# Kernel optimization log

Measured on AMD Instinct MI355X. Metric: run time of the kernel, lower is better.

## Reference

```python
import jax, jax.numpy as jnp
import numpy as np

SEQ_LEN, N_VARS, N_SKILLS, D_IN = 120, 9, 32, 1
BATCH = 32768


def setup_inputs() -> dict:
    key = jax.random.key(0)
    ks = jax.random.split(key, 8)
    H, D = N_SKILLS, D_IN
    s = 1.0 / np.sqrt(H)  # torch LSTMCell init scale
    return {
        "x": jax.random.normal(ks[0], (BATCH, N_VARS * SEQ_LEN), dtype=jnp.float32),
        # nn.LSTMCell params (gate order i,f,g,o)
        "W_ih": jax.random.uniform(ks[1], (4 * H, D), jnp.float32, -s, s),
        "W_hh": jax.random.uniform(ks[2], (4 * H, H), jnp.float32, -s, s),
        "b_ih": jax.random.uniform(ks[3], (4 * H,), jnp.float32, -s, s),
        "b_hh": jax.random.uniform(ks[4], (4 * H,), jnp.float32, -s, s),
        # contextual gate params: cg_w Linear(D,H,bias=False), cg_u Linear(H,H)
        "cg_w": jax.random.uniform(ks[5], (H, D), jnp.float32, -s, s),
        "cg_u": jax.random.uniform(ks[6], (H, H), jnp.float32, -s, s),
        "cg_b": jax.random.uniform(ks[7], (H,), jnp.float32, -s, s),
    }


def reference(x, W_ih, W_hh, b_ih, b_hh, cg_w, cg_u, cg_b):
    B = x.shape[0]
    H = N_SKILLS
    # [B, V*T] -> fold the 9 independent variable-sequences into the batch dim
    # (the same cell weights are shared across vars), then scan over time.
    xs = x.reshape(B * N_VARS, SEQ_LEN, D_IN)
    xs = jnp.moveaxis(xs, 1, 0)  # [T, B*V, D_IN]

    def step(carry, xt):
        h, c = carry  # each [B*V, H]
        gates = xt @ W_ih.T + b_ih + h @ W_hh.T + b_hh  # [B*V, 4H]
        i, f, g, o = jnp.split(gates, 4, axis=-1)
        i = jax.nn.sigmoid(i)
        f = jax.nn.sigmoid(f)
        g = jnp.tanh(g)
        c_new = f * c + i * g
        # contextual gate uses the *previous* h
        cg = jax.nn.sigmoid(xt @ cg_w.T + h @ cg_u.T + cg_b)
        h_new = cg * jnp.tanh(c_new)
        return (h_new, c_new), None

    zeros = jnp.zeros((B * N_VARS, H), dtype=x.dtype)
    (h, _), _ = jax.lax.scan(step, (zeros, zeros), xs)
    # [B*V, H] -> [B, V*H] (variable-major, matching torch.cat over vars)
    return h.reshape(B, N_VARS * H)
```

## Files before the change

### kernel.cpp

```cpp
#include <hip/hip_runtime.h>


#define NV 9
#define TLEN 120
#define HS 32
#define BATCH_ 32768
#define NSEQ (BATCH_ * NV)
#define NBATCH (NSEQ / 16)
#define WPB 4
#define GRID_ (NBATCH / (WPB * 2))

#define TCHUNK 60
#define XSTRIDE 20
#define HSTRIDE 36

#define LOG2E 1.4426950408889634f
#define TWOL  2.8853900817779268f

typedef __attribute__((ext_vector_type(8))) short bf16x8;
typedef __attribute__((ext_vector_type(4))) float f32x4;
typedef __attribute__((ext_vector_type(4))) unsigned int u32x4;

__device__ __forceinline__ float fast_exp2(float x) { return __builtin_amdgcn_exp2f(x); }
__device__ __forceinline__ float fast_rcp(float x)  { return __builtin_amdgcn_rcpf(x); }
__device__ __forceinline__ unsigned int fbits(float x) { return __builtin_bit_cast(unsigned int, x); }
__device__ __forceinline__ float bcastf(unsigned int x) { return __builtin_bit_cast(float, x); }

__device__ __forceinline__ f32x4 splat4(float x) { f32x4 v = {x, x, x, x}; return v; }
__device__ __forceinline__ f32x4 fma4(f32x4 a, f32x4 b, f32x4 c) {
  return __builtin_elementwise_fma(a, b, c);
}
__device__ __forceinline__ f32x4 exp24(f32x4 v) {
  f32x4 r;
  r[0] = fast_exp2(v[0]); r[1] = fast_exp2(v[1]);
  r[2] = fast_exp2(v[2]); r[3] = fast_exp2(v[3]);
  return r;
}
__device__ __forceinline__ f32x4 rcp4(f32x4 v) {
  f32x4 r;
  r[0] = fast_rcp(v[0]); r[1] = fast_rcp(v[1]);
  r[2] = fast_rcp(v[2]); r[3] = fast_rcp(v[3]);
  return r;
}

__device__ __forceinline__ void lstm_elem(f32x4 ai, f32x4 af, f32x4 ag, f32x4 ac,
                                          f32x4& ct, f32x4& h) {
  const f32x4 one4 = splat4(1.0f);
  f32x4 Ei = exp24(ai), Ef = exp24(af), Eg = exp24(ag), Ea = exp24(ac);
  f32x4 pi_ = Ei + one4, pf_ = Ef + one4, pg_ = Eg + one4, pa_ = Ea + one4;
  f32x4 u   = fma4(Eg, splat4(TWOL), splat4(-TWOL));
  f32x4 P   = pi_ * pg_;
  f32x4 tt  = pf_ * u;
  f32x4 num = fma4(ct, P, tt);
  f32x4 den = pf_ * P;
  ct = num * rcp4(den);
  f32x4 Ec  = exp24(ct);
  h = (one4 - Ec) * rcp4(pa_ * (Ec + one4));
}

__device__ __forceinline__ void gates8(const unsigned int* __restrict__ hb,
                                       const float* __restrict__ xTw, int tl,
                                       int col, int quad,
                                       const bf16x8 (&bhi)[8], const bf16x8 (&blo)[8],
                                       const float (&wx)[8], const float (&bb)[8],
                                       f32x4 (&acc)[8]) {
  f32x4 xt4 = *(const f32x4*)&xTw[tl * XSTRIDE + quad * 4];
#pragma unroll
  for (int tile = 0; tile < 8; ++tile)
    acc[tile] = fma4(splat4(wx[tile]), xt4, splat4(bb[tile]));
  const unsigned int* hrow = &hb[col * HSTRIDE + quad * 8];
  u32x4 wa = *(const u32x4*)hrow;
  u32x4 wz = *(const u32x4*)(hrow + 4);
  u32x4 hi4, lo4;
  hi4[0] = __builtin_amdgcn_perm(wa[1], wa[0], 0x05040100u);
  hi4[1] = __builtin_amdgcn_perm(wa[3], wa[2], 0x05040100u);
  hi4[2] = __builtin_amdgcn_perm(wz[1], wz[0], 0x05040100u);
  hi4[3] = __builtin_amdgcn_perm(wz[3], wz[2], 0x05040100u);
  lo4[0] = __builtin_amdgcn_perm(wa[1], wa[0], 0x07060302u);
  lo4[1] = __builtin_amdgcn_perm(wa[3], wa[2], 0x07060302u);
  lo4[2] = __builtin_amdgcn_perm(wz[1], wz[0], 0x07060302u);
  lo4[3] = __builtin_amdgcn_perm(wz[3], wz[2], 0x07060302u);
  bf16x8 ahi = __builtin_bit_cast(bf16x8, hi4);
  bf16x8 alo = __builtin_bit_cast(bf16x8, lo4);
#pragma unroll
  for (int tile = 0; tile < 8; ++tile) {
    acc[tile] = __builtin_amdgcn_mfma_f32_16x16x32_bf16(ahi, bhi[tile], acc[tile], 0, 0, 0);
    acc[tile] = __builtin_amdgcn_mfma_f32_16x16x32_bf16(alo, bhi[tile], acc[tile], 0, 0, 0);
    acc[tile] = __builtin_amdgcn_mfma_f32_16x16x32_bf16(ahi, blo[tile], acc[tile], 0, 0, 0);
  }
}

__device__ __forceinline__ void finish8(unsigned int* __restrict__ hb, int col, int quad,
                                        f32x4 (&acc)[8],
                                        f32x4& ct0, f32x4& ct1, f32x4& h0, f32x4& h1) {
  lstm_elem(acc[0], acc[2], acc[4], acc[6], ct0, h0);
  lstm_elem(acc[1], acc[3], acc[5], acc[7], ct1, h1);
#pragma unroll
  for (int r = 0; r < 4; ++r) {
    unsigned int hbits = fbits(h0[r]);
    float lof = h0[r] - bcastf(hbits & 0xffff0000u);
    hb[(quad * 4 + r) * HSTRIDE + col] =
        __builtin_amdgcn_perm(fbits(lof), hbits, 0x07060302u);
    unsigned int hbits1 = fbits(h1[r]);
    float lof1 = h1[r] - bcastf(hbits1 & 0xffff0000u);
    hb[(quad * 4 + r) * HSTRIDE + col + 16] =
        __builtin_amdgcn_perm(fbits(lof1), hbits1, 0x07060302u);
  }
}

__global__ __launch_bounds__(256, 2) void cglstm_kernel(
    const float* __restrict__ x,
    const float* __restrict__ W_ih,
    const float* __restrict__ W_hh,
    const float* __restrict__ b_ih,
    const float* __restrict__ b_hh,
    const float* __restrict__ cg_w,
    const float* __restrict__ cg_u,
    const float* __restrict__ cg_b,
    float* __restrict__ out)
{
  const int lane = threadIdx.x & 63;
  const int wid  = threadIdx.x >> 6;
  const int col  = lane & 15;
  const int quad = lane >> 4;

  __shared__ __align__(16) float xT[WPB][2][TCHUNK * XSTRIDE];
  __shared__ __align__(16) unsigned int hbuf[WPB][2][16 * HSTRIDE];
  float* __restrict__ xTw0 = xT[wid][0];
  float* __restrict__ xTw1 = xT[wid][1];
  unsigned int* hb0 = hbuf[wid][0];
  unsigned int* hb1 = hbuf[wid][1];

  bf16x8 bhi[8], blo[8];
  float wx[8], bb[8];
#pragma unroll
  for (int tile = 0; tile < 8; ++tile) {
    const int n = col + (tile & 1) * 16;
    const float sc_ = ((tile >> 1) == 2) ? -TWOL : -LOG2E;
    const float* wrow = (tile < 6) ? (W_hh + (size_t)((tile >> 1) * HS + n) * HS)
                                   : (cg_u + (size_t)n * HS);
    bf16x8 vh, vl;
#pragma unroll
    for (int e = 0; e < 8; ++e) {
      float wv = wrow[quad * 8 + e] * sc_;
      unsigned int wbits = fbits(wv);
      float lo_f = wv - bcastf(wbits & 0xffff0000u);
      vh[e] = (short)(wbits >> 16);
      vl[e] = (short)(fbits(lo_f) >> 16);
    }
    bhi[tile] = vh; blo[tile] = vl;
    if (tile < 6) {
      const int gg = tile >> 1;
      wx[tile] = W_ih[gg * HS + n] * sc_;
      bb[tile] = (b_ih[gg * HS + n] + b_hh[gg * HS + n]) * sc_;
    } else {
      wx[tile] = cg_w[n] * sc_;
      bb[tile] = cg_b[n] * sc_;
    }
  }

  const int p0 = (blockIdx.x * WPB + wid) * 2;
  const int p1 = p0 + 1;
  const float4* xb0 = (const float4*)(x + (size_t)p0 * 16 * TLEN);
  const float4* xb1 = (const float4*)(x + (size_t)p1 * 16 * TLEN);

  for (int i = lane; i < 2 * 16 * HSTRIDE; i += 64) hb0[i] = 0u;
  f32x4 cA0 = splat4(0.f), cA1 = splat4(0.f), hA0 = splat4(0.f), hA1 = splat4(0.f);
  f32x4 cB0 = splat4(0.f), cB1 = splat4(0.f), hB0 = splat4(0.f), hB1 = splat4(0.f);

#pragma unroll 1
  for (int chunk = 0; chunk < 2; ++chunk) {
    for (int i = lane; i < 240; i += 64) {
      int s = i / 15;
      int j = i - s * 15;
      float4 v = xb0[s * 30 + chunk * 15 + j];
      int t0 = j * 4;
      xTw0[(t0 + 0) * XSTRIDE + s] = v.x;
      xTw0[(t0 + 1) * XSTRIDE + s] = v.y;
      xTw0[(t0 + 2) * XSTRIDE + s] = v.z;
      xTw0[(t0 + 3) * XSTRIDE + s] = v.w;
    }
    for (int i = lane; i < 240; i += 64) {
      int s = i / 15;
      int j = i - s * 15;
      float4 v = xb1[s * 30 + chunk * 15 + j];
      int t0 = j * 4;
      xTw1[(t0 + 0) * XSTRIDE + s] = v.x;
      xTw1[(t0 + 1) * XSTRIDE + s] = v.y;
      xTw1[(t0 + 2) * XSTRIDE + s] = v.z;
      xTw1[(t0 + 3) * XSTRIDE + s] = v.w;
    }

#pragma unroll 1
    for (int tl = 0; tl < TCHUNK; ++tl) {
      f32x4 acc0[8], acc1[8];
      gates8(hb0, xTw0, tl, col, quad, bhi, blo, wx, bb, acc0);
      gates8(hb1, xTw1, tl, col, quad, bhi, blo, wx, bb, acc1);
      finish8(hb0, col, quad, acc0, cA0, cA1, hA0, hA1);
      finish8(hb1, col, quad, acc1, cB0, cB1, hB0, hB1);
    }
  }

  float* ob0 = out + (size_t)p0 * 16 * HS;
  float* ob1 = out + (size_t)p1 * 16 * HS;
#pragma unroll
  for (int r = 0; r < 4; ++r) {
    ob0[(quad * 4 + r) * HS + col]      = hA0[r];
    ob0[(quad * 4 + r) * HS + col + 16] = hA1[r];
    ob1[(quad * 4 + r) * HS + col]      = hB0[r];
    ob1[(quad * 4 + r) * HS + col + 16] = hB1[r];
  }
}

extern "C" void kernel_launch(void* const* d_in, const int* in_sizes, int n_in,
                              void* d_out, int out_size, void* d_ws, size_t ws_size,
                              hipStream_t stream) {
  const float* x    = (const float*)d_in[0];
  const float* W_ih = (const float*)d_in[1];
  const float* W_hh = (const float*)d_in[2];
  const float* b_ih = (const float*)d_in[3];
  const float* b_hh = (const float*)d_in[4];
  const float* cg_w = (const float*)d_in[5];
  const float* cg_u = (const float*)d_in[6];
  const float* cg_b = (const float*)d_in[7];
  float* out = (float*)d_out;

  dim3 grid(GRID_), block(256);
  hipLaunchKernelGGL(cglstm_kernel, grid, block, 0, stream,
                     x, W_ih, W_hh, b_ih, b_hh, cg_w, cg_u, cg_b, out);
}
```

Baseline: 1.370 ms.

## Software-pipeline the two sequence groups so MFMA overlaps the other group's activations

Each wave carries two independent 16-sequence groups through the recurrence. The step loop is restructured so the MFMA gate products for one group are interleaved with the exp/rcp activation math and h packing of the other group, with a prologue and epilogue per chunk. The intent is to hide MFMA latency behind transcendental VALU work instead of running all gates before all finishes. The cost is more live accumulator registers (two sets of eight f32x4), which could pressure occupancy under launch_bounds(256,2), and it relies on the compiler keeping the hand-written interleave order.

```diff
diff --git a/kernel.cpp b/kernel.cpp
--- a/kernel.cpp
+++ b/kernel.cpp
@@ -41,6 +41,17 @@
   r[0] = fast_rcp(v[0]); r[1] = fast_rcp(v[1]);
   r[2] = fast_rcp(v[2]); r[3] = fast_rcp(v[3]);
   return r;
+}
+
+__device__ __forceinline__ void pack_h(unsigned int* __restrict__ hb, int base_col,
+                                       int quad, const f32x4& h) {
+#pragma unroll
+  for (int r = 0; r < 4; ++r) {
+    unsigned int hbits = fbits(h[r]);
+    float lof = h[r] - bcastf(hbits & 0xffff0000u);
+    hb[(quad * 4 + r) * HSTRIDE + base_col] =
+        __builtin_amdgcn_perm(fbits(lof), hbits, 0x07060302u);
+  }
 }
 
 __device__ __forceinline__ void lstm_elem(f32x4 ai, f32x4 af, f32x4 ag, f32x4 ac,
@@ -95,17 +106,80 @@
                                         f32x4& ct0, f32x4& ct1, f32x4& h0, f32x4& h1) {
   lstm_elem(acc[0], acc[2], acc[4], acc[6], ct0, h0);
   lstm_elem(acc[1], acc[3], acc[5], acc[7], ct1, h1);
-#pragma unroll
-  for (int r = 0; r < 4; ++r) {
-    unsigned int hbits = fbits(h0[r]);
-    float lof = h0[r] - bcastf(hbits & 0xffff0000u);
-    hb[(quad * 4 + r) * HSTRIDE + col] =
-        __builtin_amdgcn_perm(fbits(lof), hbits, 0x07060302u);
-    unsigned int hbits1 = fbits(h1[r]);
-    float lof1 = h1[r] - bcastf(hbits1 & 0xffff0000u);
-    hb[(quad * 4 + r) * HSTRIDE + col + 16] =
-        __builtin_amdgcn_perm(fbits(lof1), hbits1, 0x07060302u);
-  }
+  pack_h(hb, col, quad, h0);
+  pack_h(hb, col + 16, quad, h1);
+}
+
+#define MFMA3(T)                                                                        \
+  accX[T] = __builtin_amdgcn_mfma_f32_16x16x32_bf16(ahi, bhi[T], accX[T], 0, 0, 0);     \
+  accX[T] = __builtin_amdgcn_mfma_f32_16x16x32_bf16(alo, bhi[T], accX[T], 0, 0, 0);     \
+  accX[T] = __builtin_amdgcn_mfma_f32_16x16x32_bf16(ahi, blo[T], accX[T], 0, 0, 0);
+
+__device__ __forceinline__ void fused_step(
+    const unsigned int* __restrict__ hbX, const float* __restrict__ xTX, int tlX,
+    f32x4 (&accX)[8],
+    unsigned int* __restrict__ hbY, f32x4 (&accY)[8],
+    f32x4& cY0, f32x4& cY1, f32x4& hY0, f32x4& hY1,
+    int col, int quad,
+    const bf16x8 (&bhi)[8], const bf16x8 (&blo)[8],
+    const float (&wx)[8], const float (&bb)[8])
+{
+  const f32x4 one4 = splat4(1.0f);
+  f32x4 xt4 = *(const f32x4*)&xTX[tlX * XSTRIDE + quad * 4];
+#pragma unroll
+  for (int t = 0; t < 8; ++t)
+    accX[t] = fma4(splat4(wx[t]), xt4, splat4(bb[t]));
+  const unsigned int* hrow = &hbX[col * HSTRIDE + quad * 8];
+  u32x4 wa = *(const u32x4*)hrow;
+  u32x4 wz = *(const u32x4*)(hrow + 4);
+  u32x4 hi4, lo4;
+  hi4[0] = __builtin_amdgcn_perm(wa[1], wa[0], 0x05040100u);
+  hi4[1] = __builtin_amdgcn_perm(wa[3], wa[2], 0x05040100u);
+  hi4[2] = __builtin_amdgcn_perm(wz[1], wz[0], 0x05040100u);
+  hi4[3] = __builtin_amdgcn_perm(wz[3], wz[2], 0x05040100u);
+  lo4[0] = __builtin_amdgcn_perm(wa[1], wa[0], 0x07060302u);
+  lo4[1] = __builtin_amdgcn_perm(wa[3], wa[2], 0x07060302u);
+  lo4[2] = __builtin_amdgcn_perm(wz[1], wz[0], 0x07060302u);
+  lo4[3] = __builtin_amdgcn_perm(wz[3], wz[2], 0x07060302u);
+  bf16x8 ahi = __builtin_bit_cast(bf16x8, hi4);
+  bf16x8 alo = __builtin_bit_cast(bf16x8, lo4);
+
+  MFMA3(0)
+  f32x4 Ei0 = exp24(accY[0]);
+  f32x4 Ef0 = exp24(accY[2]);
+  MFMA3(1)
+  f32x4 Eg0 = exp24(accY[4]);
+  f32x4 Ea0 = exp24(accY[6]);
+  MFMA3(2)
+  f32x4 pi0 = Ei0 + one4, pf0 = Ef0 + one4, pg0 = Eg0 + one4, pa0 = Ea0 + one4;
+  f32x4 u0   = fma4(Eg0, splat4(TWOL), splat4(-TWOL));
+  f32x4 P0   = pi0 * pg0;
+  f32x4 tt0  = pf0 * u0;
+  f32x4 num0 = fma4(cY0, P0, tt0);
+  f32x4 den0 = pf0 * P0;
+  MFMA3(3)
+  cY0 = num0 * rcp4(den0);
+  f32x4 Ec0 = exp24(cY0);
+  hY0 = (one4 - Ec0) * rcp4(pa0 * (Ec0 + one4));
+  MFMA3(4)
+  pack_h(hbY, col, quad, hY0);
+  f32x4 Ei1 = exp24(accY[1]);
+  f32x4 Ef1 = exp24(accY[3]);
+  MFMA3(5)
+  f32x4 Eg1 = exp24(accY[5]);
+  f32x4 Ea1 = exp24(accY[7]);
+  MFMA3(6)
+  f32x4 pi1 = Ei1 + one4, pf1 = Ef1 + one4, pg1 = Eg1 + one4, pa1 = Ea1 + one4;
+  f32x4 u1   = fma4(Eg1, splat4(TWOL), splat4(-TWOL));
+  f32x4 P1   = pi1 * pg1;
+  f32x4 tt1  = pf1 * u1;
+  f32x4 num1 = fma4(cY1, P1, tt1);
+  f32x4 den1 = pf1 * P1;
+  MFMA3(7)
+  cY1 = num1 * rcp4(den1);
+  f32x4 Ec1 = exp24(cY1);
+  hY1 = (one4 - Ec1) * rcp4(pa1 * (Ec1 + one4));
+  pack_h(hbY, col + 16, quad, hY1);
 }
 
 __global__ __launch_bounds__(256, 2) void cglstm_kernel(
@@ -167,6 +241,7 @@
   for (int i = lane; i < 2 * 16 * HSTRIDE; i += 64) hb0[i] = 0u;
   f32x4 cA0 = splat4(0.f), cA1 = splat4(0.f), hA0 = splat4(0.f), hA1 = splat4(0.f);
   f32x4 cB0 = splat4(0.f), cB1 = splat4(0.f), hB0 = splat4(0.f), hB1 = splat4(0.f);
+  f32x4 accA[8], accB[8];
 
 #pragma unroll 1
   for (int chunk = 0; chunk < 2; ++chunk) {
@@ -191,14 +266,17 @@
       xTw1[(t0 + 3) * XSTRIDE + s] = v.w;
     }
 
+    gates8(hb0, xTw0, 0, col, quad, bhi, blo, wx, bb, accA);
 #pragma unroll 1
-    for (int tl = 0; tl < TCHUNK; ++tl) {
-      f32x4 acc0[8], acc1[8];
-      gates8(hb0, xTw0, tl, col, quad, bhi, blo, wx, bb, acc0);
-      gates8(hb1, xTw1, tl, col, quad, bhi, blo, wx, bb, acc1);
-      finish8(hb0, col, quad, acc0, cA0, cA1, hA0, hA1);
-      finish8(hb1, col, quad, acc1, cB0, cB1, hB0, hB1);
-    }
+    for (int tl = 0; tl < TCHUNK - 1; ++tl) {
+      fused_step(hb1, xTw1, tl, accB, hb0, accA, cA0, cA1, hA0, hA1,
+                 col, quad, bhi, blo, wx, bb);
+      fused_step(hb0, xTw0, tl + 1, accA, hb1, accB, cB0, cB1, hB0, hB1,
+                 col, quad, bhi, blo, wx, bb);
+    }
+    fused_step(hb1, xTw1, TCHUNK - 1, accB, hb0, accA, cA0, cA1, hA0, hA1,
+               col, quad, bhi, blo, wx, bb);
+    finish8(hb1, col, quad, accB, cB0, cB1, hB0, hB1);
   }
 
   float* ob0 = out + (size_t)p0 * 16 * HS;
```

Measured after the change: 1.331 ms, median of 2. 1.03x faster.
